# Optimization experiments

Measured on AMD Instinct MI355X. Metric: run time of the kernel, lower is better.

## Reference

```python
import jax, jax.numpy as jnp
import numpy as np

NL, D, Di, N, R, K, V, NH = 24, 768, 1536, 16, 48, 4, 50280, 12
BATCH, SEQ = 4, 256


def setup_inputs():
    key = jax.random.key(0)
    it = iter(jax.random.split(key, 48))
    g = lambda shape, s=0.02: jax.random.normal(next(it), shape, jnp.float32) * s
    inp = {
        "question_ids": jax.random.randint(next(it), (BATCH, SEQ), 0, V),
        "question_mask": jnp.ones((BATCH, SEQ), jnp.int32),
        "answer_ids": jax.random.randint(next(it), (BATCH, SEQ), 0, V),
        "answer_mask": jnp.ones((BATCH, SEQ), jnp.int32),
        "embed": g((V, D)),
        "norm_w": jnp.ones((NL, D)),
        "in_proj_w": g((NL, 2 * Di, D)),
        "conv_w": g((NL, Di, K), 0.1),
        "conv_b": jnp.zeros((NL, Di)),
        "x_proj_w": g((NL, R + 2 * N, Di)),
        "dt_proj_w": g((NL, Di, R)),
        "dt_proj_b": g((NL, Di), 0.5) - 4.0,
        "A_log": jnp.log(jnp.broadcast_to(jnp.arange(1, N + 1, dtype=jnp.float32), (NL, Di, N))) + 0.0,
        "D_p": jnp.ones((NL, Di)),
        "out_proj_w": g((NL, D, Di)),
        "norm_f": jnp.ones((D,)),
        "ln1_w": jnp.ones((D,)), "ln1_b": jnp.zeros((D,)),
        "qkv_w": g((3 * D, D)), "qkv_b": jnp.zeros((3 * D,)),
        "attn_out_w": g((D, D)), "attn_out_b": jnp.zeros((D,)),
        "ln2_w": jnp.ones((D,)), "ln2_b": jnp.zeros((D,)),
        "ff1_w": g((4 * D, D)), "ff1_b": jnp.zeros((4 * D,)),
        "ff2_w": g((D, 4 * D)), "ff2_b": jnp.zeros((D,)),
        "C_w": g((1, N)), "proj_out_w": g((D, Di)),
        "B_w": g((N, 1)), "proj_in_w": g((Di, D), 0.002),
    }
    return inp


def _rms(x, w, eps=1e-5):
    return x * jax.lax.rsqrt(jnp.mean(x * x, axis=-1, keepdims=True) + eps) * w


def _ln(x, w, b, eps=1e-5):
    m = jnp.mean(x, axis=-1, keepdims=True)
    v = jnp.var(x, axis=-1, keepdims=True)
    return (x - m) * jax.lax.rsqrt(v + eps) * w + b


def _mamba_block(h, layer, init_state):
    nw, ipw, cw, cb, xpw, dpw, dpb, alog, dp, opw = layer
    x_in = _rms(h, nw)
    xz = jnp.einsum('bld,ed->ble', x_in, ipw)  # (B,L,2*Di)
    x, z = jnp.split(xz, 2, axis=-1)
    L = x.shape[1]
    xp = jnp.pad(x, ((0, 0), (K - 1, 0), (0, 0)))  # causal depthwise conv, kernel K
    x = sum(xp[:, k:k + L, :] * cw[:, k] for k in range(K)) + cb
    x = jax.nn.silu(x)
    dbl = jnp.einsum('bld,ed->ble', x, xpw)
    dt, Bm, Cm = dbl[..., :R], dbl[..., R:R + N], dbl[..., R + N:]
    delta = jax.nn.softplus(jnp.einsum('blr,dr->bld', dt, dpw) + dpb)  # (B,L,Di)
    A = -jnp.exp(alog)  # (Di,N)

    def step(hs, t):  # selective scan, carry (B,Di,N)
        d_t, x_t, B_t, C_t = t
        hs = jnp.exp(d_t[..., None] * A) * hs + (d_t * x_t)[..., None] * B_t[:, None, :]
        return hs, jnp.einsum('bdn,bn->bd', hs, C_t)

    xs = tuple(jnp.moveaxis(a, 1, 0) for a in (delta, x, Bm, Cm))
    last, ys = jax.lax.scan(step, init_state, xs)
    y = jnp.moveaxis(ys, 0, 1) + x * dp
    y = y * jax.nn.silu(z)
    return h + jnp.einsum('bld,od->blo', y, opw), last


def _backbone(ids, mask, embed, mamba_params, norm_f, init_states):
    h = embed[ids] * mask[..., None].astype(embed.dtype)
    block = jax.checkpoint(_mamba_block)  # remat per layer: bounds bwd memory

    def layer_step(carry, xs):
        *layer, st = xs
        return block(carry, tuple(layer), st)

    h, lasts = jax.lax.scan(layer_step, h, mamba_params + (init_states,))
    h = _rms(h, norm_f)
    return jnp.einsum('bld,vd->blv', h, embed), lasts  # tied lm head


def _tf_layer(x, ln1_w, ln1_b, qkv_w, qkv_b, attn_out_w, attn_out_b, ln2_w, ln2_b, ff1_w, ff1_b, ff2_w, ff2_b):
    B, S, _ = x.shape
    hd = D // NH
    y = _ln(x, ln1_w, ln1_b)  # norm_first pre-LN
    q, k, v = jnp.split(y @ qkv_w.T + qkv_b, 3, axis=-1)
    q = q.reshape(B, S, NH, hd); k = k.reshape(B, S, NH, hd); v = v.reshape(B, S, NH, hd)
    att = jax.nn.softmax(jnp.einsum('bqhd,bkhd->bhqk', q, k) / jnp.sqrt(jnp.float32(hd)), axis=-1)
    o = jnp.einsum('bhqk,bkhd->bqhd', att, v).reshape(B, S, D)
    x = x + o @ attn_out_w.T + attn_out_b
    y = _ln(x, ln2_w, ln2_b)
    return x + jax.nn.gelu(y @ ff1_w.T + ff1_b, approximate=False) @ ff2_w.T + ff2_b


def _refine(states, C_w, proj_out_w, B_w, proj_in_w, tf_params):
    # states: (B, NL, Di, N); 12-step recurrent state refinement
    for _ in range(12):
        d = jnp.einsum('bsdn,n->bsd', states, C_w[0])  # C: Linear(16,1), squeeze(-1)
        d = jnp.einsum('bsd,od->bso', d, proj_out_w)   # 1536 -> 768
        d = _tf_layer(d, *tf_params)
        d = jnp.einsum('bso,do->bsd', d, proj_in_w)    # 768 -> 1536
        states = states + d[..., None] * B_w[:, 0]     # B: Linear(1,16)
    return states


def reference(question_ids, question_mask, answer_ids, answer_mask, embed, norm_w, in_proj_w, conv_w, conv_b, x_proj_w, dt_proj_w, dt_proj_b, A_log, D_p, out_proj_w, norm_f, ln1_w, ln1_b, qkv_w, qkv_b, attn_out_w, attn_out_b, ln2_w, ln2_b, ff1_w, ff1_b, ff2_w, ff2_b, C_w, proj_out_w, B_w, proj_in_w):
    mamba_params = (norm_w, in_proj_w, conv_w, conv_b, x_proj_w, dt_proj_w, dt_proj_b, A_log, D_p, out_proj_w)
    tf_params = (ln1_w, ln1_b, qkv_w, qkv_b, attn_out_w, attn_out_b, ln2_w, ln2_b, ff1_w, ff1_b, ff2_w, ff2_b)
    Bsz = question_ids.shape[0]
    zeros = jnp.zeros((NL, Bsz, Di, N), embed.dtype)
    _, lasts = _backbone(question_ids, question_mask, embed, mamba_params, norm_f, zeros)
    states = jnp.moveaxis(lasts, 0, 1)  # torch.stack(states, dim=1): (B, NL, Di, N)
    states = _refine(states, C_w, proj_out_w, B_w, proj_in_w, tf_params)
    logits, _ = _backbone(answer_ids, answer_mask, embed, mamba_params, norm_f, jnp.moveaxis(states, 0, 1))
    return logits
```

## Files before the change

### kernel.cpp

```cpp
#include <hip/hip_runtime.h>
#include <math.h>

namespace {

constexpr int kNL = 24, kD = 768, kDi = 1536, kN = 16, kR = 48, kK = 4, kV = 50280, kNH = 12;
constexpr int kB = 4, kS = 256;
constexpr int kMtok = kB * kS;
constexpr int kMref = kB * kNL;
constexpr int kVp = 50304;

using bf16x8   = __attribute__((ext_vector_type(8))) short;
using f32x4    = __attribute__((ext_vector_type(4))) float;
using ushort8v = __attribute__((ext_vector_type(8))) unsigned short;

__device__ __forceinline__ float siluf(float x) { return x / (1.f + __expf(-x)); }

__device__ __forceinline__ ushort f2b(float f) {
    union { float f; unsigned u; } v; v.f = f;
    unsigned u = v.u;
    unsigned r = (u + 0x7FFFu + ((u >> 16) & 1u)) >> 16;
    return (ushort)r;
}
__device__ __forceinline__ float b2f(ushort u) {
    union { unsigned u; float f; } v; v.u = (unsigned)u << 16; return v.f;
}

#define GLOAD_LDS(g, l) \
    __builtin_amdgcn_global_load_lds((const __attribute__((address_space(1))) void*)(g), \
                                     (__attribute__((address_space(3))) void*)(l), 16, 0, 0)

template <int BM, int BN, int BIAS, int ACT, int RES, int OUTMODE, int PIPE, int SSQ = 0>
__global__ __launch_bounds__(256, (PIPE == 3 ? 3 : 2)) void gemm_bf16(
    const ushort* __restrict__ A, int lda,
    const ushort* __restrict__ B, int ldb,
    float* __restrict__ C, int ldc,
    ushort* __restrict__ Cbf, int ldcb,
    float* __restrict__ C2,
    const float* __restrict__ bias,
    const float* __restrict__ aux,
    int M, int N, int K)
{
    constexpr int ACH = BM / 32;
    constexpr int BCH = BN / 32;
    constexpr int MI  = BM / 32;
    constexpr int NJ  = BN / 32;

    __shared__ ushort As[PIPE][BM * 64];
    __shared__ ushort Bs[PIPE][BN * 64];

    const int tid  = threadIdx.x;
    const int lane = tid & 63;
    const int wave = tid >> 6;
    const int m0 = blockIdx.y * BM;
    const int n0 = blockIdx.x * BN;
    const int wr = (wave >> 1) * (BM / 2);
    const int wc = (wave & 1) * (BN / 2);

    f32x4 acc[MI][NJ];
#pragma unroll
    for (int i = 0; i < MI; ++i)
#pragma unroll
        for (int j = 0; j < NJ; ++j) acc[i][j] = f32x4{0.f, 0.f, 0.f, 0.f};

    const int srow = lane >> 3;
    const int scol = ((lane & 7) ^ srow) * 8;
    const ushort* gA[ACH];
    const ushort* gB[BCH];
#pragma unroll
    for (int g = 0; g < ACH; ++g)
        gA[g] = A + (size_t)(m0 + (g * 4 + wave) * 8 + srow) * lda + scol;
#pragma unroll
    for (int g = 0; g < BCH; ++g)
        gB[g] = B + (size_t)(n0 + (g * 4 + wave) * 8 + srow) * ldb + scol;

    const int frow = lane & 15;
    const int kh   = lane >> 4;
    const int nt   = K >> 6;

    auto stage = [&](int t, int buf) {
        const int off = t * 64;
#pragma unroll
        for (int g = 0; g < ACH; ++g) GLOAD_LDS(gA[g] + off, &As[buf][(g * 4 + wave) * 512]);
#pragma unroll
        for (int g = 0; g < BCH; ++g) GLOAD_LDS(gB[g] + off, &Bs[buf][(g * 4 + wave) * 512]);
    };
    auto compute = [&](int buf) {
#pragma unroll
        for (int s = 0; s < 2; ++s) {
            bf16x8 fa[MI], fb[NJ];
#pragma unroll
            for (int i = 0; i < MI; ++i) {
                int r = wr + i * 16 + frow;
                int slot = (s * 4 + kh) ^ (r & 7);
                fa[i] = *(const bf16x8*)&As[buf][r * 64 + slot * 8];
            }
#pragma unroll
            for (int j = 0; j < NJ; ++j) {
                int r = wc + j * 16 + frow;
                int slot = (s * 4 + kh) ^ (r & 7);
                fb[j] = *(const bf16x8*)&Bs[buf][r * 64 + slot * 8];
            }
#pragma unroll
            for (int i = 0; i < MI; ++i)
#pragma unroll
                for (int j = 0; j < NJ; ++j)
                    acc[i][j] = __builtin_amdgcn_mfma_f32_16x16x32_bf16(fa[i], fb[j], acc[i][j], 0, 0, 0);
        }
    };

    if constexpr (PIPE == 3) {
        stage(0, 0);
        if (nt > 1) stage(1, 1);
        for (int t = 0; t < nt; ++t) {
            if (t < nt - 1) {
                asm volatile("s_waitcnt vmcnt(%0)" :: "n"(ACH + BCH) : "memory");
            } else {
                asm volatile("s_waitcnt vmcnt(0)" ::: "memory");
            }
            __builtin_amdgcn_s_barrier();
            if (t + 2 < nt) stage(t + 2, (t + 2) % 3);
            compute(t % 3);
        }
        __builtin_amdgcn_s_barrier();
    } else {
        stage(0, 0);
        __syncthreads();
        int cur = 0;
        for (int t = 0; t < nt; ++t) {
            if (t + 1 < nt) stage(t + 1, cur ^ 1);
            compute(cur);
            __syncthreads();
            cur ^= 1;
        }
    }

    const int ccol = lane & 15;
    const int crow = (lane >> 4) * 4;
    float rsq[MI][4];
    if constexpr (SSQ) {
#pragma unroll
        for (int i = 0; i < MI; ++i)
#pragma unroll
            for (int q = 0; q < 4; ++q) rsq[i][q] = 0.f;
    }
#pragma unroll
    for (int i = 0; i < MI; ++i) {
#pragma unroll
        for (int j = 0; j < NJ; ++j) {
            int gn = n0 + wc + j * 16 + ccol;
            if (gn >= N) continue;
            float bv = BIAS ? bias[gn] : 0.f;
#pragma unroll
            for (int q = 0; q < 4; ++q) {
                int gm = m0 + wr + i * 16 + crow + q;
                if (gm >= M) continue;
                float v = acc[i][j][q] + bv;
                if (ACT == 1) v = fmaxf(v, 0.f) + log1pf(expf(-fabsf(v)));
                if (ACT == 2) v = 0.5f * v * (1.f + erff(v * 0.70710678118654752f));
                if (OUTMODE == 3) {
                    if (gn < 48) Cbf[(size_t)gm * 64 + gn] = f2b(v);
                    else if (gn < 64) { Cbf[(size_t)gm * 64 + gn] = 0; C2[(size_t)(gn - 48) * kMtok + gm] = v; }
                    else if (gn < 80) C2[(size_t)(gn - 48) * kMtok + gm] = v;
                } else if (OUTMODE == 4) {
                    ((ushort*)C2)[(size_t)gn * kMtok + gm] = f2b(v);
                } else if (OUTMODE == 7) {
                    int bb = gm / kNL, ss = gm - bb * kNL;
                    float* stp = C2 + ((size_t)(ss * kB + bb) * kDi + gn) * kN;
                    float a2 = 0.f;
#pragma unroll
                    for (int nn = 0; nn < kN; ++nn) {
                        float sv = stp[nn] + v * bias[nn];
                        stp[nn] = sv;
                        a2 += sv * aux[nn];
                    }
                    Cbf[(size_t)gm * ldcb + gn] = f2b(a2);
                } else {
                    size_t ci = (size_t)gm * ldc + gn;
                    if (RES) v += C[ci];
                    if (OUTMODE != 2) C[ci] = v;
                    if (OUTMODE == 1 || OUTMODE == 2) Cbf[(size_t)gm * ldcb + gn] = f2b(v);
                    if constexpr (SSQ) rsq[i][q] += v * v;
                }
            }
        }
    }
    if constexpr (SSQ) {
#pragma unroll
        for (int i = 0; i < MI; ++i)
#pragma unroll
            for (int q = 0; q < 4; ++q) {
                rsq[i][q] += __shfl_xor(rsq[i][q], 1, 16);
                rsq[i][q] += __shfl_xor(rsq[i][q], 2, 16);
                rsq[i][q] += __shfl_xor(rsq[i][q], 4, 16);
                rsq[i][q] += __shfl_xor(rsq[i][q], 8, 16);
            }
        float* red = (float*)&As[0][0];
        __syncthreads();
        if ((lane & 15) == 0) {
#pragma unroll
            for (int i = 0; i < MI; ++i)
#pragma unroll
                for (int q = 0; q < 4; ++q) {
                    int rl = (wave >> 1) * 32 + i * 16 + (lane >> 4) * 4 + q;
                    red[(wave & 1) * 64 + rl] = rsq[i][q];
                }
        }
        __syncthreads();
        if (tid < 64) C2[(size_t)blockIdx.x * kMtok + m0 + tid] = red[tid] + red[64 + tid];
    }
}

template <int BM, int BN, int BIAS, int ACT, int RES, int OUTMODE, int PIPE, int SSQ = 0>
static void gemm(const ushort* A, int lda, const ushort* B, int ldb,
                 float* C, int ldc, ushort* Cb, int ldcb, float* C2,
                 const float* bias, const float* aux, int M, int N, int K, hipStream_t s)
{
    dim3 g((N + BN - 1) / BN, (M + BM - 1) / BM);
    gemm_bf16<BM, BN, BIAS, ACT, RES, OUTMODE, PIPE, SSQ><<<g, dim3(256), 0, s>>>(
        A, lda, B, ldb, C, ldc, Cb, ldcb, C2, bias, aux, M, N, K);
}

__global__ __launch_bounds__(256, 4) void gemm_rms(
    const float* __restrict__ hbuf, const float* __restrict__ ssq,
    const float* __restrict__ nw,
    const ushort* __restrict__ B, int ldb,
    ushort* __restrict__ Xbf, ushort* __restrict__ zTb,
    int M, int N, int K)
{
    constexpr int MI = 2, NJ = 2, BCH = 2;
    __shared__ ushort As[2][64 * 64];
    __shared__ ushort Bs[2][64 * 64];
    const int tid  = threadIdx.x;
    const int lane = tid & 63;
    const int wave = tid >> 6;
    const int m0 = blockIdx.y * 64;
    const int n0 = blockIdx.x * 64;
    const int wr = (wave >> 1) * 32;
    const int wc = (wave & 1) * 32;

    f32x4 acc[MI][NJ];
#pragma unroll
    for (int i = 0; i < MI; ++i)
#pragma unroll
        for (int j = 0; j < NJ; ++j) acc[i][j] = f32x4{0.f, 0.f, 0.f, 0.f};

    const int srow = lane >> 3;
    const int scol = ((lane & 7) ^ srow) * 8;
    const ushort* gB[BCH];
#pragma unroll
    for (int g = 0; g < BCH; ++g)
        gB[g] = B + (size_t)(n0 + (g * 4 + wave) * 8 + srow) * ldb + scol;

    int arow[2];
    float rs[2];
#pragma unroll
    for (int g = 0; g < 2; ++g) {
        arow[g] = m0 + (g * 4 + wave) * 8 + srow;
        float s = 0.f;
#pragma unroll
        for (int c = 0; c < 12; ++c) s += ssq[c * kMtok + arow[g]];
        rs[g] = rsqrtf(s * (1.f / 768.f) + 1e-5f);
    }

    const int frow = lane & 15;
    const int kh   = lane >> 4;
    const int nt   = K >> 6;

    float4 av[2][2], wv[2];
    auto loadA = [&](int t) {
        int k = t * 64 + scol;
        wv[0] = *(const float4*)&nw[k];
        wv[1] = *(const float4*)&nw[k + 4];
#pragma unroll
        for (int g = 0; g < 2; ++g) {
            av[g][0] = *(const float4*)&hbuf[(size_t)arow[g] * K + k];
            av[g][1] = *(const float4*)&hbuf[(size_t)arow[g] * K + k + 4];
        }
    };
    auto writeA = [&](int buf) {
#pragma unroll
        for (int g = 0; g < 2; ++g) {
            ushort8v o;
            o[0] = f2b(av[g][0].x * rs[g] * wv[0].x);
            o[1] = f2b(av[g][0].y * rs[g] * wv[0].y);
            o[2] = f2b(av[g][0].z * rs[g] * wv[0].z);
            o[3] = f2b(av[g][0].w * rs[g] * wv[0].w);
            o[4] = f2b(av[g][1].x * rs[g] * wv[1].x);
            o[5] = f2b(av[g][1].y * rs[g] * wv[1].y);
            o[6] = f2b(av[g][1].z * rs[g] * wv[1].z);
            o[7] = f2b(av[g][1].w * rs[g] * wv[1].w);
            *(ushort8v*)&As[buf][(g * 4 + wave) * 512 + lane * 8] = o;
        }
    };
    auto stageB = [&](int t, int buf) {
#pragma unroll
        for (int g = 0; g < BCH; ++g) GLOAD_LDS(gB[g] + t * 64, &Bs[buf][(g * 4 + wave) * 512]);
    };
    auto compute = [&](int buf) {
#pragma unroll
        for (int s = 0; s < 2; ++s) {
            bf16x8 fa[MI], fb[NJ];
#pragma unroll
            for (int i = 0; i < MI; ++i) {
                int r = wr + i * 16 + frow;
                int slot = (s * 4 + kh) ^ (r & 7);
                fa[i] = *(const bf16x8*)&As[buf][r * 64 + slot * 8];
            }
#pragma unroll
            for (int j = 0; j < NJ; ++j) {
                int r = wc + j * 16 + frow;
                int slot = (s * 4 + kh) ^ (r & 7);
                fb[j] = *(const bf16x8*)&Bs[buf][r * 64 + slot * 8];
            }
#pragma unroll
            for (int i = 0; i < MI; ++i)
#pragma unroll
                for (int j = 0; j < NJ; ++j)
                    acc[i][j] = __builtin_amdgcn_mfma_f32_16x16x32_bf16(fa[i], fb[j], acc[i][j], 0, 0, 0);
        }
    };

    loadA(0);
    stageB(0, 0);
    writeA(0);
    __syncthreads();
    int cur = 0;
    for (int t = 0; t < nt; ++t) {
        if (t + 1 < nt) { loadA(t + 1); stageB(t + 1, cur ^ 1); }
        compute(cur);
        if (t + 1 < nt) writeA(cur ^ 1);
        __syncthreads();
        cur ^= 1;
    }

    const int ccol = lane & 15;
    const int crow = (lane >> 4) * 4;
#pragma unroll
    for (int i = 0; i < MI; ++i) {
#pragma unroll
        for (int j = 0; j < NJ; ++j) {
            int gn = n0 + wc + j * 16 + ccol;
#pragma unroll
            for (int q = 0; q < 4; ++q) {
                int gm = m0 + wr + i * 16 + crow + q;
                float v = acc[i][j][q];
                if (gn < kDi) Xbf[(size_t)gm * kDi + gn] = f2b(v);
                else zTb[(size_t)(gn - kDi) * kMtok + gm] = f2b(siluf(v));
            }
        }
    }
}

__global__ void cvt_kernel(const float* __restrict__ src, ushort* __restrict__ dst, int n) {
    int i = (blockIdx.x * 256 + threadIdx.x) * 4;
    if (i >= n) return;
    float4 v = *(const float4*)(src + i);
    ushort4 o; o.x = f2b(v.x); o.y = f2b(v.y); o.z = f2b(v.z); o.w = f2b(v.w);
    *(ushort4*)(dst + i) = o;
}

__global__ void cvt_xpw_kernel(const float* __restrict__ src, ushort* __restrict__ dst) {
    int i = (blockIdx.x * 256 + threadIdx.x) * 4;
    if (i >= 24 * 80 * 1536) return;
    int l = i / (80 * 1536), r = i - l * (80 * 1536);
    int row = r / 1536, col = r - row * 1536;
    float4 v = *(const float4*)(src + i);
    ushort4 o; o.x = f2b(v.x); o.y = f2b(v.y); o.z = f2b(v.z); o.w = f2b(v.w);
    *(ushort4*)(dst + ((size_t)(l * 128 + row)) * 1536 + col) = o;
}

__global__ void cvt_dpw_kernel(const float* __restrict__ src, ushort* __restrict__ dst) {
    int i = blockIdx.x * 256 + threadIdx.x;
    if (i >= 24 * 1536 * 64) return;
    int col = i & 63, row = i >> 6;
    dst[i] = (col < 48) ? f2b(src[(size_t)row * 48 + col]) : (ushort)0;
}

__global__ void embed_kernel(const int* __restrict__ ids, const int* __restrict__ msk,
                             const float* __restrict__ embed, float* __restrict__ h,
                             float* __restrict__ ssq)
{
    int i = blockIdx.x * 256 + threadIdx.x;
    int row = i / kD, col = i - row * kD;
    float v = embed[(size_t)ids[row] * kD + col] * (float)msk[row];
    h[i] = v;
    float s = v * v;
    s += __shfl_xor(s, 1);  s += __shfl_xor(s, 2);  s += __shfl_xor(s, 4);
    s += __shfl_xor(s, 8);  s += __shfl_xor(s, 16); s += __shfl_xor(s, 32);
    if ((threadIdx.x & 63) == 0) ssq[(col >> 6) * kMtok + row] = s;
}

__global__ __launch_bounds__(256) void rms_kernel(const float* __restrict__ x,
                                                  const float* __restrict__ w,
                                                  ushort* __restrict__ out)
{
    __shared__ float red[256];
    int row = blockIdx.x, tid = threadIdx.x;
    const float* xr = x + (size_t)row * kD;
    float s = 0.f;
    for (int j = tid; j < kD; j += 256) { float v = xr[j]; s += v * v; }
    red[tid] = s; __syncthreads();
    for (int o = 128; o > 0; o >>= 1) { if (tid < o) red[tid] += red[tid + o]; __syncthreads(); }
    float rs = rsqrtf(red[0] / (float)kD + 1e-5f);
    for (int j = tid; j < kD; j += 256) out[(size_t)row * kD + j] = f2b(xr[j] * rs * w[j]);
}

__global__ __launch_bounds__(256) void ln_kernel(const float* __restrict__ x,
                                                 const float* __restrict__ w,
                                                 const float* __restrict__ b,
                                                 ushort* __restrict__ out)
{
    __shared__ float r1[256], r2[256];
    int row = blockIdx.x, tid = threadIdx.x;
    const float* xr = x + (size_t)row * kD;
    float s = 0.f, s2 = 0.f;
    for (int j = tid; j < kD; j += 256) { float v = xr[j]; s += v; s2 += v * v; }
    r1[tid] = s; r2[tid] = s2; __syncthreads();
    for (int o = 128; o > 0; o >>= 1) {
        if (tid < o) { r1[tid] += r1[tid + o]; r2[tid] += r2[tid + o]; }
        __syncthreads();
    }
    float mean = r1[0] / (float)kD;
    float var = r2[0] / (float)kD - mean * mean;
    float rsv = rsqrtf(var + 1e-5f);
    for (int j = tid; j < kD; j += 256)
        out[(size_t)row * kD + j] = f2b((xr[j] - mean) * rsv * w[j] + b[j]);
}

__global__ __launch_bounds__(256) void conv_kernel(
    const ushort* __restrict__ xb, const float* __restrict__ cw,
    const float* __restrict__ cb, ushort* __restrict__ xc_bf,
    ushort* __restrict__ xcT)
{
    int d   = blockIdx.x * 256 + threadIdx.x;
    int bt0 = blockIdx.y * 16;
    int t0  = bt0 & (kS - 1);
    float w0 = cw[d * 4], w1 = cw[d * 4 + 1], w2 = cw[d * 4 + 2], w3 = cw[d * 4 + 3];
    float bias = cb[d];
    float xv[19];
#pragma unroll
    for (int j = 0; j < 19; ++j) {
        int tt = t0 - 3 + j;
        xv[j] = (tt >= 0) ? b2f(xb[(size_t)(bt0 - 3 + j) * kDi + d]) : 0.f;
    }
    ushort8v o0, o1;
#pragma unroll
    for (int e = 0; e < 16; ++e) {
        float s = bias + xv[e] * w0 + xv[e + 1] * w1 + xv[e + 2] * w2 + xv[e + 3] * w3;
        ushort us = f2b(siluf(s));
        xc_bf[(size_t)(bt0 + e) * kDi + d] = us;
        if (e < 8) o0[e] = us; else o1[e - 8] = us;
    }
    *(ushort8v*)(xcT + (size_t)d * kMtok + bt0)     = o0;
    *(ushort8v*)(xcT + (size_t)d * kMtok + bt0 + 8) = o1;
}

__global__ __launch_bounds__(256) void scan_kernel(
    const ushort* __restrict__ dltT, const ushort* __restrict__ xcT,
    const ushort* __restrict__ zT, const float* __restrict__ bcT,
    const float* __restrict__ alog, const float* __restrict__ dp,
    float* __restrict__ states, ushort* __restrict__ y)
{
    int gid = blockIdx.x * 256 + threadIdx.x;
    int n = gid & 15;
    int d = (gid >> 4) % kDi;
    int b = gid / (kDi * kN);
    float Areg = -__expf(alog[d * kN + n]);
    float dpv = dp[d];
    size_t sidx = (size_t)(b * kDi + d) * kN + n;
    float hs = states[sidx];
    const ushort8v* pD = (const ushort8v*)(dltT + (size_t)d * kMtok + b * kS);
    const ushort8v* pX = (const ushort8v*)(xcT  + (size_t)d * kMtok + b * kS);
    const ushort8v* pZ = (const ushort8v*)(zT   + (size_t)d * kMtok + b * kS);
    const float4* pB = (const float4*)(bcT + (size_t)n * kMtok + b * kS);
    const float4* pC = (const float4*)(bcT + (size_t)(16 + n) * kMtok + b * kS);
    ushort8v D = pD[0], X = pX[0], Z = pZ[0];
    float4 B0 = pB[0], B1 = pB[1], C0 = pC[0], C1 = pC[1];
    ushort* yrow = y + (size_t)(b * kS) * kDi + d;
    for (int g = 0; g < kS / 8; ++g) {
        ushort8v Dn, Xn, Zn; float4 Bn0, Bn1, Cn0, Cn1;
        if (g + 1 < kS / 8) {
            Dn = pD[g + 1]; Xn = pX[g + 1]; Zn = pZ[g + 1];
            Bn0 = pB[2 * g + 2]; Bn1 = pB[2 * g + 3];
            Cn0 = pC[2 * g + 2]; Cn1 = pC[2 * g + 3];
        }
#pragma unroll
        for (int e = 0; e < 8; ++e) {
            float dv = b2f(D[e]), xv = b2f(X[e]), zv = b2f(Z[e]);
            float Bv = (e < 4) ? (&B0.x)[e] : (&B1.x)[e - 4];
            float Cv = (e < 4) ? (&C0.x)[e] : (&C1.x)[e - 4];
            hs = __expf(dv * Areg) * hs + (dv * xv) * Bv;
            float p = hs * Cv;
            p += __shfl_xor(p, 1, 16);
            p += __shfl_xor(p, 2, 16);
            p += __shfl_xor(p, 4, 16);
            p += __shfl_xor(p, 8, 16);
            if (n == 0) yrow[(size_t)(g * 8 + e) * kDi] = f2b((p + xv * dpv) * zv);
        }
        D = Dn; X = Xn; Z = Zn; B0 = Bn0; B1 = Bn1; C0 = Cn0; C1 = Cn1;
    }
    states[sidx] = hs;
}

__global__ void contract_kernel(const float* __restrict__ st, const float* __restrict__ Cw,
                                ushort* __restrict__ dDi)
{
    int i = blockIdx.x * 256 + threadIdx.x;
    int row = i / kDi, di = i - row * kDi;
    int b = row / kNL, s = row - b * kNL;
    const float* sp = st + ((size_t)(s * kB + b) * kDi + di) * kN;
    float acc = 0.f;
#pragma unroll
    for (int nn = 0; nn < kN; ++nn) acc += sp[nn] * Cw[nn];
    dDi[i] = f2b(acc);
}

__global__ __launch_bounds__(32) void attn_kernel(const float* __restrict__ qkv,
                                                  ushort* __restrict__ o)
{
    int b = blockIdx.x / kNH;
    int hh = blockIdx.x - b * kNH;
    int sq = threadIdx.x;
    if (sq >= kNL) return;
    const float* qrow = qkv + (size_t)(b * kNL + sq) * (3 * kD) + hh * 64;
    float q[64];
#pragma unroll
    for (int e = 0; e < 64; ++e) q[e] = qrow[e];
    float sc[kNL];
    float mx = -1e30f;
    for (int sk = 0; sk < kNL; ++sk) {
        const float* krow = qkv + (size_t)(b * kNL + sk) * (3 * kD) + kD + hh * 64;
        float dt = 0.f;
#pragma unroll
        for (int e = 0; e < 64; ++e) dt += q[e] * krow[e];
        dt *= 0.125f;
        sc[sk] = dt;
        mx = fmaxf(mx, dt);
    }
    float sum = 0.f;
    for (int sk = 0; sk < kNL; ++sk) { sc[sk] = expf(sc[sk] - mx); sum += sc[sk]; }
    float inv = 1.f / sum;
    float out[64];
#pragma unroll
    for (int e = 0; e < 64; ++e) out[e] = 0.f;
    for (int sk = 0; sk < kNL; ++sk) {
        float wgt = sc[sk] * inv;
        const float* vrow = qkv + (size_t)(b * kNL + sk) * (3 * kD) + 2 * kD + hh * 64;
#pragma unroll
        for (int e = 0; e < 64; ++e) out[e] += wgt * vrow[e];
    }
    ushort* orow = o + (size_t)(b * kNL + sq) * kD + hh * 64;
#pragma unroll
    for (int e = 0; e < 64; ++e) orow[e] = f2b(out[e]);
}

}

extern "C" void kernel_launch(void* const* d_in, const int* in_sizes, int n_in,
                              void* d_out, int out_size, void* d_ws, size_t ws_size,
                              hipStream_t stream)
{
    const int*   q_ids  = (const int*)d_in[0];
    const int*   q_msk  = (const int*)d_in[1];
    const int*   a_ids  = (const int*)d_in[2];
    const int*   a_msk  = (const int*)d_in[3];
    const float* embed  = (const float*)d_in[4];
    const float* norm_w = (const float*)d_in[5];
    const float* ipw    = (const float*)d_in[6];
    const float* cw     = (const float*)d_in[7];
    const float* cb     = (const float*)d_in[8];
    const float* xpw    = (const float*)d_in[9];
    const float* dpw    = (const float*)d_in[10];
    const float* dpb    = (const float*)d_in[11];
    const float* alog   = (const float*)d_in[12];
    const float* dpp    = (const float*)d_in[13];
    const float* opw    = (const float*)d_in[14];
    const float* norm_f = (const float*)d_in[15];
    const float* ln1w   = (const float*)d_in[16];
    const float* ln1b   = (const float*)d_in[17];
    const float* qkvw   = (const float*)d_in[18];
    const float* qkvbi  = (const float*)d_in[19];
    const float* aow    = (const float*)d_in[20];
    const float* aob    = (const float*)d_in[21];
    const float* ln2w   = (const float*)d_in[22];
    const float* ln2b   = (const float*)d_in[23];
    const float* ff1w   = (const float*)d_in[24];
    const float* ff1b   = (const float*)d_in[25];
    const float* ff2w   = (const float*)d_in[26];
    const float* ff2b   = (const float*)d_in[27];
    const float* Cwp    = (const float*)d_in[28];
    const float* powp   = (const float*)d_in[29];
    const float* Bwp    = (const float*)d_in[30];
    const float* piwp   = (const float*)d_in[31];

    char* base = (char*)d_ws;
    size_t cur = 0;
    auto allocB = [&](size_t bytes) { char* p = base + cur; cur = (cur + bytes + 255) & ~(size_t)255; return p; };
    auto allocF = [&](size_t n) { return (float*)allocB(n * 4); };
    auto allocH = [&](size_t n) { return (ushort*)allocB(n * 2); };

    float* h     = allocF((size_t)kMtok * kD);
    float* ssqp  = allocF((size_t)12 * kMtok);
    float* bcT   = allocF((size_t)32 * kMtok);
    float* st    = allocF((size_t)kNL * kB * kDi * kN);
    float* x768  = allocF((size_t)kMref * kD);
    float* qkvB  = allocF((size_t)kMref * 3 * kD);
    ushort* x_bf    = allocH((size_t)kMtok * kDi);
    ushort* zT_b    = allocH((size_t)kDi * kMtok);
    ushort* xcT_b   = allocH((size_t)kDi * kMtok);
    ushort* dltT_b  = allocH((size_t)kDi * kMtok);
    ushort* xc_bf   = allocH((size_t)kMtok * kDi);
    ushort* dtin_bf = allocH((size_t)kMtok * 64);
    ushort* yb_bf   = allocH((size_t)kMtok * kDi);
    ushort* xin_bf  = allocH((size_t)kMtok * kD);
    ushort* dDi_bf  = allocH((size_t)128 * kDi);
    ushort* tb_bf   = allocH((size_t)128 * kD);
    ushort* o768_bf = allocH((size_t)128 * kD);
    ushort* f3_bf   = allocH((size_t)128 * 4 * kD);
    ushort* x768_bf = allocH((size_t)128 * kD);
    ushort* xpw_bf  = allocH((size_t)kNL * 128 * kDi);
    ushort* dpw_bf  = allocH((size_t)kNL * kDi * 64);
    ushort* powp_bf = allocH((size_t)kD * kDi);
    ushort* qkvw_bf = allocH((size_t)3 * kD * kD);
    ushort* aow_bf  = allocH((size_t)kD * kD);
    ushort* ff1w_bf = allocH((size_t)4 * kD * kD);
    ushort* ff2w_bf = allocH((size_t)kD * 4 * kD);
    ushort* piw_bf  = allocH((size_t)kDi * kD);
    ushort* emb_bf  = allocH((size_t)kVp * kD);

    size_t base_end = cur;
    ushort* ipw_all = allocH((size_t)kNL * 2 * kDi * kD);
    ushort* opw_all = allocH((size_t)kNL * kD * kDi);
    bool full = (cur <= ws_size);
    ushort* ipw_stg = nullptr;
    ushort* opw_stg = nullptr;
    if (!full) {
        cur = base_end;
        ipw_stg = allocH((size_t)2 * kDi * kD);
        opw_stg = allocH((size_t)kD * kDi);
        if (cur > ws_size) return;
    }

    auto cvt = [&](const float* s, ushort* d, size_t n) {
        cvt_kernel<<<dim3((unsigned)((n / 4 + 255) / 256)), dim3(256), 0, stream>>>(s, d, (int)n);
    };

    hipMemsetAsync(st, 0, sizeof(float) * (size_t)kNL * kB * kDi * kN, stream);

    cvt_xpw_kernel<<<dim3(2880), dim3(256), 0, stream>>>(xpw, xpw_bf);
    cvt_dpw_kernel<<<dim3(9216), dim3(256), 0, stream>>>(dpw, dpw_bf);
    cvt(powp, powp_bf, (size_t)kD * kDi);
    cvt(qkvw, qkvw_bf, (size_t)3 * kD * kD);
    cvt(aow,  aow_bf,  (size_t)kD * kD);
    cvt(ff1w, ff1w_bf, (size_t)4 * kD * kD);
    cvt(ff2w, ff2w_bf, (size_t)kD * 4 * kD);
    cvt(piwp, piw_bf,  (size_t)kDi * kD);
    cvt(embed, emb_bf, (size_t)kV * kD);
    if (full) {
        cvt(ipw, ipw_all, (size_t)kNL * 2 * kDi * kD);
        cvt(opw, opw_all, (size_t)kNL * kD * kDi);
    }

    for (int pass = 0; pass < 2; ++pass) {
        const int* ids = pass ? a_ids : q_ids;
        const int* msk = pass ? a_msk : q_msk;

        embed_kernel<<<dim3(kMtok * kD / 256), dim3(256), 0, stream>>>(ids, msk, embed, h, ssqp);

        for (int l = 0; l < kNL; ++l) {
            const ushort* ipw_l;
            const ushort* opw_l;
            if (full) {
                ipw_l = ipw_all + (size_t)l * 2 * kDi * kD;
                opw_l = opw_all + (size_t)l * kD * kDi;
            } else {
                cvt(ipw + (size_t)l * 2 * kDi * kD, ipw_stg, (size_t)2 * kDi * kD);
                cvt(opw + (size_t)l * kD * kDi, opw_stg, (size_t)kD * kDi);
                ipw_l = ipw_stg;
                opw_l = opw_stg;
            }
            gemm_rms<<<dim3(48, 16), dim3(256), 0, stream>>>(
                h, ssqp, norm_w + (size_t)l * kD, ipw_l, kD, x_bf, zT_b, kMtok, 2 * kDi, kD);
            conv_kernel<<<dim3(kDi / 256, kMtok / 16), dim3(256), 0, stream>>>(
                x_bf, cw + (size_t)l * kDi * kK, cb + (size_t)l * kDi, xc_bf, xcT_b);
            gemm<64, 64, 0, 0, 0, 3, 3>(xc_bf, kDi, xpw_bf + (size_t)l * 128 * kDi, kDi,
                                        nullptr, 0, dtin_bf, 0, bcT,
                                        nullptr, nullptr, kMtok, 128, kDi, stream);
            gemm<64, 64, 1, 1, 0, 4, 3>(dtin_bf, 64, dpw_bf + (size_t)l * kDi * 64, 64,
                                        nullptr, 0, nullptr, 0, (float*)dltT_b,
                                        dpb + (size_t)l * kDi, nullptr, kMtok, kDi, 64, stream);
            scan_kernel<<<dim3(kB * kDi * kN / 256), dim3(256), 0, stream>>>(
                dltT_b, xcT_b, zT_b, bcT, alog + (size_t)l * kDi * kN, dpp + (size_t)l * kDi,
                st + (size_t)l * kB * kDi * kN, yb_bf);
            gemm<64, 64, 0, 0, 1, 0, 3, 1>(yb_bf, kDi, opw_l, kDi, h, kD, nullptr, 0, ssqp,
                                           nullptr, nullptr, kMtok, kD, kDi, stream);
        }

        if (pass == 0) {
            contract_kernel<<<dim3(kMref * kDi / 256), dim3(256), 0, stream>>>(st, Cwp, dDi_bf);
            for (int it = 0; it < 12; ++it) {
                gemm<64, 64, 0, 0, 0, 0, 3>(dDi_bf, kDi, powp_bf, kDi, x768, kD, nullptr, 0, nullptr,
                                            nullptr, nullptr, kMref, kD, kDi, stream);
                ln_kernel<<<dim3(kMref), dim3(256), 0, stream>>>(x768, ln1w, ln1b, tb_bf);
                gemm<64, 64, 1, 0, 0, 0, 3>(tb_bf, kD, qkvw_bf, kD, qkvB, 3 * kD, nullptr, 0, nullptr,
                                            qkvbi, nullptr, kMref, 3 * kD, kD, stream);
                attn_kernel<<<dim3(kB * kNH), dim3(32), 0, stream>>>(qkvB, o768_bf);
                gemm<64, 64, 1, 0, 1, 0, 3>(o768_bf, kD, aow_bf, kD, x768, kD, nullptr, 0, nullptr,
                                            aob, nullptr, kMref, kD, kD, stream);
                ln_kernel<<<dim3(kMref), dim3(256), 0, stream>>>(x768, ln2w, ln2b, tb_bf);
                gemm<64, 64, 1, 2, 0, 2, 3>(tb_bf, kD, ff1w_bf, kD, nullptr, 0, f3_bf, 4 * kD, nullptr,
                                            ff1b, nullptr, kMref, 4 * kD, kD, stream);
                gemm<64, 64, 1, 0, 1, 1, 3>(f3_bf, 4 * kD, ff2w_bf, 4 * kD, x768, kD, x768_bf, kD, nullptr,
                                            ff2b, nullptr, kMref, kD, 4 * kD, stream);
                gemm<64, 64, 0, 0, 0, 7, 3>(x768_bf, kD, piw_bf, kD, nullptr, 0, dDi_bf, kDi, st,
                                            Bwp, Cwp, kMref, kDi, kD, stream);
            }
        } else {
            rms_kernel<<<dim3(kMtok), dim3(256), 0, stream>>>(h, norm_f, xin_bf);
            gemm<128, 128, 0, 0, 0, 0, 2>(xin_bf, kD, emb_bf, kD, (float*)d_out, kV, nullptr, 0, nullptr,
                                          nullptr, nullptr, kMtok, kV, kD, stream);
        }
    }
}
```

Before: 8.637 ms.

## Fuse conv, x_proj and dt_proj into one kernel; fold ff2 into proj_in

Adds a per-layer prep kernel that computes the causal conv with SiLU and the x_proj GEMM, then the dt_proj GEMM with softplus, all in one launch. This removes the conv_kernel and two GEMM launches along with their intermediate global buffers. In the refine loop it precomputes proj_in·ff2 and its bias offline and concatenates the activations into one wide K=3840 operand, so the ff2 GEMM and the proj_in GEMM become a single GEMM. The prep kernel launches only 32 blocks, which may underuse the GPU, and the folded weights change bf16 rounding.

```diff
diff --git a/kernel.cpp b/kernel.cpp
--- a/kernel.cpp
+++ b/kernel.cpp
@@ -8,6 +8,7 @@
 constexpr int kMtok = kB * kS;
 constexpr int kMref = kB * kNL;
 constexpr int kVp = 50304;
+constexpr int kKa = 3840;
 
 using bf16x8   = __attribute__((ext_vector_type(8))) short;
 using f32x4    = __attribute__((ext_vector_type(4))) float;
@@ -38,6 +39,7 @@
     float* __restrict__ C2,
     const float* __restrict__ bias,
     const float* __restrict__ aux,
+    const float* __restrict__ aux2,
     int M, int N, int K)
 {
     constexpr int ACH = BM / 32;
@@ -157,19 +159,13 @@
                 float v = acc[i][j][q] + bv;
                 if (ACT == 1) v = fmaxf(v, 0.f) + log1pf(expf(-fabsf(v)));
                 if (ACT == 2) v = 0.5f * v * (1.f + erff(v * 0.70710678118654752f));
-                if (OUTMODE == 3) {
-                    if (gn < 48) Cbf[(size_t)gm * 64 + gn] = f2b(v);
-                    else if (gn < 64) { Cbf[(size_t)gm * 64 + gn] = 0; C2[(size_t)(gn - 48) * kMtok + gm] = v; }
-                    else if (gn < 80) C2[(size_t)(gn - 48) * kMtok + gm] = v;
-                } else if (OUTMODE == 4) {
-                    ((ushort*)C2)[(size_t)gn * kMtok + gm] = f2b(v);
-                } else if (OUTMODE == 7) {
+                if (OUTMODE == 7) {
                     int bb = gm / kNL, ss = gm - bb * kNL;
                     float* stp = C2 + ((size_t)(ss * kB + bb) * kDi + gn) * kN;
                     float a2 = 0.f;
 #pragma unroll
                     for (int nn = 0; nn < kN; ++nn) {
-                        float sv = stp[nn] + v * bias[nn];
+                        float sv = stp[nn] + v * aux2[nn];
                         stp[nn] = sv;
                         a2 += sv * aux[nn];
                     }
@@ -213,11 +209,12 @@
 template <int BM, int BN, int BIAS, int ACT, int RES, int OUTMODE, int PIPE, int SSQ = 0>
 static void gemm(const ushort* A, int lda, const ushort* B, int ldb,
                  float* C, int ldc, ushort* Cb, int ldcb, float* C2,
-                 const float* bias, const float* aux, int M, int N, int K, hipStream_t s)
+                 const float* bias, const float* aux, int M, int N, int K, hipStream_t s,
+                 const float* aux2 = nullptr)
 {
     dim3 g((N + BN - 1) / BN, (M + BM - 1) / BM);
     gemm_bf16<BM, BN, BIAS, ACT, RES, OUTMODE, PIPE, SSQ><<<g, dim3(256), 0, s>>>(
-        A, lda, B, ldb, C, ldc, Cb, ldcb, C2, bias, aux, M, N, K);
+        A, lda, B, ldb, C, ldc, Cb, ldcb, C2, bias, aux, aux2, M, N, K);
 }
 
 __global__ __launch_bounds__(256, 4) void gemm_rms(
@@ -351,6 +348,205 @@
     }
 }
 
+__global__ __launch_bounds__(256, 2) void prep_kernel(
+    const ushort* __restrict__ xb,
+    const float* __restrict__ cw,
+    const float* __restrict__ cb,
+    const ushort* __restrict__ xpw128,
+    const ushort* __restrict__ dpw64,
+    const float* __restrict__ dpb,
+    ushort* __restrict__ xcT,
+    float*  __restrict__ bcT,
+    ushort* __restrict__ dltT)
+{
+    __shared__ ushort lds[2 * 32 * 64 + 2 * 128 * 64];
+    ushort* As1 = lds;
+    ushort* Bs1 = lds + 4096;
+    ushort* dtL = lds;
+    ushort* Bs2 = lds + 4096;
+
+    const int tid  = threadIdx.x;
+    const int lane = tid & 63;
+    const int wave = tid >> 6;
+    const int m0   = blockIdx.x * 32;
+
+    f32x4 acc[2][2];
+#pragma unroll
+    for (int i = 0; i < 2; ++i)
+#pragma unroll
+        for (int j = 0; j < 2; ++j) acc[i][j] = f32x4{0.f, 0.f, 0.f, 0.f};
+
+    const int srow = lane >> 3;
+    const int scol8 = ((lane & 7) ^ srow) * 8;
+    const int frow = lane & 15;
+    const int kh   = lane >> 4;
+    const int ccol = lane & 15;
+    const int crow = (lane >> 4) * 4;
+
+    const int ar = tid >> 3;
+    const int acg = tid & 7;
+    const int gt = m0 + ar;
+    const int tloc = gt & (kS - 1);
+
+    ushort8v xrow[4];
+    float4 w4[8];
+    float cbv[8];
+    auto loadA = [&](int t) {
+        int gcol = t * 64 + ((acg ^ (ar & 7)) << 3);
+#pragma unroll
+        for (int j = 0; j < 4; ++j) {
+            int tt = tloc - 3 + j;
+            if (tt >= 0) xrow[j] = *(const ushort8v*)&xb[(size_t)(gt - 3 + j) * kDi + gcol];
+            else { ushort8v z; for (int e = 0; e < 8; ++e) z[e] = 0; xrow[j] = z; }
+        }
+#pragma unroll
+        for (int e = 0; e < 8; ++e) w4[e] = *(const float4*)&cw[(size_t)(gcol + e) * 4];
+        float4 c0 = *(const float4*)&cb[gcol];
+        float4 c1 = *(const float4*)&cb[gcol + 4];
+        cbv[0] = c0.x; cbv[1] = c0.y; cbv[2] = c0.z; cbv[3] = c0.w;
+        cbv[4] = c1.x; cbv[5] = c1.y; cbv[6] = c1.z; cbv[7] = c1.w;
+    };
+    auto writeA = [&](int buf) {
+        ushort8v o;
+#pragma unroll
+        for (int e = 0; e < 8; ++e) {
+            float s = cbv[e] + b2f(xrow[0][e]) * w4[e].x + b2f(xrow[1][e]) * w4[e].y
+                             + b2f(xrow[2][e]) * w4[e].z + b2f(xrow[3][e]) * w4[e].w;
+            o[e] = f2b(siluf(s));
+        }
+        *(ushort8v*)&As1[buf * 2048 + ar * 64 + acg * 8] = o;
+    };
+    const ushort* gB[4];
+#pragma unroll
+    for (int g = 0; g < 4; ++g)
+        gB[g] = xpw128 + (size_t)((wave * 4 + g) * 8 + srow) * kDi + scol8;
+    auto stageB = [&](int t, int buf) {
+#pragma unroll
+        for (int g = 0; g < 4; ++g)
+            GLOAD_LDS(gB[g] + t * 64, &Bs1[buf * 8192 + (wave * 4 + g) * 512]);
+    };
+    auto compute1 = [&](int buf) {
+#pragma unroll
+        for (int s = 0; s < 2; ++s) {
+            bf16x8 fa[2], fb[2];
+#pragma unroll
+            for (int i = 0; i < 2; ++i) {
+                int r = i * 16 + frow;
+                int slot = (s * 4 + kh) ^ (r & 7);
+                fa[i] = *(const bf16x8*)&As1[buf * 2048 + r * 64 + slot * 8];
+            }
+#pragma unroll
+            for (int j = 0; j < 2; ++j) {
+                int rb = wave * 32 + j * 16 + frow;
+                int slot = (s * 4 + kh) ^ (rb & 7);
+                fb[j] = *(const bf16x8*)&Bs1[buf * 8192 + rb * 64 + slot * 8];
+            }
+#pragma unroll
+            for (int i = 0; i < 2; ++i)
+#pragma unroll
+                for (int j = 0; j < 2; ++j)
+                    acc[i][j] = __builtin_amdgcn_mfma_f32_16x16x32_bf16(fa[i], fb[j], acc[i][j], 0, 0, 0);
+        }
+    };
+    auto xcTwrite = [&](int buf, int t) {
+        int d = lane;
+        ushort vals[8];
+#pragma unroll
+        for (int u = 0; u < 8; ++u) {
+            int r = wave * 8 + u;
+            vals[u] = As1[buf * 2048 + r * 64 + (((d >> 3) ^ (r & 7)) * 8) + (d & 7)];
+        }
+        ushort8v o;
+#pragma unroll
+        for (int u = 0; u < 8; ++u) o[u] = vals[u];
+        *(ushort8v*)&xcT[(size_t)(t * 64 + d) * kMtok + m0 + wave * 8] = o;
+    };
+
+    loadA(0);
+    stageB(0, 0);
+    writeA(0);
+    __syncthreads();
+    int cur = 0;
+    for (int t = 0; t < 24; ++t) {
+        if (t + 1 < 24) { loadA(t + 1); stageB(t + 1, cur ^ 1); }
+        compute1(cur);
+        xcTwrite(cur, t);
+        if (t + 1 < 24) writeA(cur ^ 1);
+        __syncthreads();
+        cur ^= 1;
+    }
+
+#pragma unroll
+    for (int i = 0; i < 2; ++i) {
+#pragma unroll
+        for (int j = 0; j < 2; ++j) {
+            int gnl = wave * 32 + j * 16 + ccol;
+#pragma unroll
+            for (int q = 0; q < 4; ++q) {
+                int rl = i * 16 + crow + q;
+                float v = acc[i][j][q];
+                if (gnl < 64)
+                    dtL[rl * 64 + (((gnl >> 3) ^ (rl & 7)) * 8) + (gnl & 7)] = (gnl < 48) ? f2b(v) : (ushort)0;
+                if (gnl >= 48 && gnl < 80)
+                    bcT[(size_t)(gnl - 48) * kMtok + m0 + rl] = v;
+            }
+        }
+    }
+    __syncthreads();
+
+    const ushort* gB2[2];
+#pragma unroll
+    for (int g = 0; g < 2; ++g)
+        gB2[g] = dpw64 + (size_t)((wave * 2 + g) * 8 + srow) * 64 + scol8;
+    auto stage2 = [&](int n, int buf) {
+#pragma unroll
+        for (int g = 0; g < 2; ++g)
+            GLOAD_LDS(gB2[g] + (size_t)n * 64 * 64, &Bs2[buf * 4096 + (wave * 2 + g) * 512]);
+    };
+
+    stage2(0, 0);
+    __syncthreads();
+    int cur2 = 0;
+    for (int n = 0; n < 24; ++n) {
+        if (n + 1 < 24) stage2(n + 1, cur2 ^ 1);
+        f32x4 a2[2];
+        a2[0] = f32x4{0.f, 0.f, 0.f, 0.f};
+        a2[1] = f32x4{0.f, 0.f, 0.f, 0.f};
+#pragma unroll
+        for (int s = 0; s < 2; ++s) {
+            bf16x8 fa[2], fb;
+#pragma unroll
+            for (int i = 0; i < 2; ++i) {
+                int r = i * 16 + frow;
+                int slot = (s * 4 + kh) ^ (r & 7);
+                fa[i] = *(const bf16x8*)&dtL[r * 64 + slot * 8];
+            }
+            int rb = wave * 16 + frow;
+            int slot = (s * 4 + kh) ^ (rb & 7);
+            fb = *(const bf16x8*)&Bs2[cur2 * 4096 + rb * 64 + slot * 8];
+#pragma unroll
+            for (int i = 0; i < 2; ++i)
+                a2[i] = __builtin_amdgcn_mfma_f32_16x16x32_bf16(fa[i], fb, a2[i], 0, 0, 0);
+        }
+#pragma unroll
+        for (int i = 0; i < 2; ++i) {
+            int gn = n * 64 + wave * 16 + ccol;
+            float bv = dpb[gn];
+            ushort ov[4];
+#pragma unroll
+            for (int q = 0; q < 4; ++q) {
+                float v = a2[i][q] + bv;
+                v = fmaxf(v, 0.f) + log1pf(expf(-fabsf(v)));
+                ov[q] = f2b(v);
+            }
+            *(ushort4*)&dltT[(size_t)gn * kMtok + m0 + i * 16 + crow] =
+                make_ushort4(ov[0], ov[1], ov[2], ov[3]);
+        }
+        __syncthreads();
+        cur2 ^= 1;
+    }
+}
+
 __global__ void cvt_kernel(const float* __restrict__ src, ushort* __restrict__ dst, int n) {
     int i = (blockIdx.x * 256 + threadIdx.x) * 4;
     if (i >= n) return;
@@ -374,6 +570,29 @@
     if (i >= 24 * 1536 * 64) return;
     int col = i & 63, row = i >> 6;
     dst[i] = (col < 48) ? f2b(src[(size_t)row * 48 + col]) : (ushort)0;
+}
+
+__global__ void cvt_ff2T_kernel(const float* __restrict__ src, ushort* __restrict__ dst) {
+    int i = blockIdx.x * 256 + threadIdx.x;
+    if (i >= 768 * 3072) return;
+    int d = i / 3072, f = i - d * 3072;
+    dst[(size_t)f * 768 + d] = f2b(src[i]);
+}
+
+__global__ void cvt_pi_kernel(const float* __restrict__ src, ushort* __restrict__ dst) {
+    int i = blockIdx.x * 256 + threadIdx.x;
+    if (i >= 1536 * 768) return;
+    int o = i / 768, d = i - o * 768;
+    dst[(size_t)o * kKa + d] = f2b(src[i]);
+}
+
+__global__ void pib_kernel(const float* __restrict__ piw, const float* __restrict__ ff2b,
+                           float* __restrict__ bias2) {
+    int o = blockIdx.x * 256 + threadIdx.x;
+    if (o >= 1536) return;
+    float s = 0.f;
+    for (int d = 0; d < 768; ++d) s += piw[(size_t)o * 768 + d] * ff2b[d];
+    bias2[o] = s;
 }
 
 __global__ void embed_kernel(const int* __restrict__ ids, const int* __restrict__ msk,
@@ -425,34 +644,6 @@
     float rsv = rsqrtf(var + 1e-5f);
     for (int j = tid; j < kD; j += 256)
         out[(size_t)row * kD + j] = f2b((xr[j] - mean) * rsv * w[j] + b[j]);
-}
-
-__global__ __launch_bounds__(256) void conv_kernel(
-    const ushort* __restrict__ xb, const float* __restrict__ cw,
-    const float* __restrict__ cb, ushort* __restrict__ xc_bf,
-    ushort* __restrict__ xcT)
-{
-    int d   = blockIdx.x * 256 + threadIdx.x;
-    int bt0 = blockIdx.y * 16;
-    int t0  = bt0 & (kS - 1);
-    float w0 = cw[d * 4], w1 = cw[d * 4 + 1], w2 = cw[d * 4 + 2], w3 = cw[d * 4 + 3];
-    float bias = cb[d];
-    float xv[19];
-#pragma unroll
-    for (int j = 0; j < 19; ++j) {
-        int tt = t0 - 3 + j;
-        xv[j] = (tt >= 0) ? b2f(xb[(size_t)(bt0 - 3 + j) * kDi + d]) : 0.f;
-    }
-    ushort8v o0, o1;
-#pragma unroll
-    for (int e = 0; e < 16; ++e) {
-        float s = bias + xv[e] * w0 + xv[e + 1] * w1 + xv[e + 2] * w2 + xv[e + 3] * w3;
-        ushort us = f2b(siluf(s));
-        xc_bf[(size_t)(bt0 + e) * kDi + d] = us;
-        if (e < 8) o0[e] = us; else o1[e - 8] = us;
-    }
-    *(ushort8v*)(xcT + (size_t)d * kMtok + bt0)     = o0;
-    *(ushort8v*)(xcT + (size_t)d * kMtok + bt0 + 8) = o1;
 }
 
 __global__ __launch_bounds__(256) void scan_kernel(
@@ -605,27 +796,26 @@
     float* st    = allocF((size_t)kNL * kB * kDi * kN);
     float* x768  = allocF((size_t)kMref * kD);
     float* qkvB  = allocF((size_t)kMref * 3 * kD);
+    float* bias2 = allocF((size_t)kDi);
     ushort* x_bf    = allocH((size_t)kMtok * kDi);
     ushort* zT_b    = allocH((size_t)kDi * kMtok);
     ushort* xcT_b   = allocH((size_t)kDi * kMtok);
     ushort* dltT_b  = allocH((size_t)kDi * kMtok);
-    ushort* xc_bf   = allocH((size_t)kMtok * kDi);
-    ushort* dtin_bf = allocH((size_t)kMtok * 64);
     ushort* yb_bf   = allocH((size_t)kMtok * kDi);
     ushort* xin_bf  = allocH((size_t)kMtok * kD);
     ushort* dDi_bf  = allocH((size_t)128 * kDi);
     ushort* tb_bf   = allocH((size_t)128 * kD);
     ushort* o768_bf = allocH((size_t)128 * kD);
-    ushort* f3_bf   = allocH((size_t)128 * 4 * kD);
-    ushort* x768_bf = allocH((size_t)128 * kD);
+    ushort* A2      = allocH((size_t)128 * kKa);
     ushort* xpw_bf  = allocH((size_t)kNL * 128 * kDi);
     ushort* dpw_bf  = allocH((size_t)kNL * kDi * 64);
     ushort* powp_bf = allocH((size_t)kD * kDi);
     ushort* qkvw_bf = allocH((size_t)3 * kD * kD);
     ushort* aow_bf  = allocH((size_t)kD * kD);
     ushort* ff1w_bf = allocH((size_t)4 * kD * kD);
-    ushort* ff2w_bf = allocH((size_t)kD * 4 * kD);
+    ushort* ff2wT   = allocH((size_t)4 * kD * kD);
     ushort* piw_bf  = allocH((size_t)kDi * kD);
+    ushort* B2      = allocH((size_t)kDi * kKa);
     ushort* emb_bf  = allocH((size_t)kVp * kD);
 
     size_t base_end = cur;
@@ -653,8 +843,12 @@
     cvt(qkvw, qkvw_bf, (size_t)3 * kD * kD);
     cvt(aow,  aow_bf,  (size_t)kD * kD);
     cvt(ff1w, ff1w_bf, (size_t)4 * kD * kD);
-    cvt(ff2w, ff2w_bf, (size_t)kD * 4 * kD);
     cvt(piwp, piw_bf,  (size_t)kDi * kD);
+    cvt_ff2T_kernel<<<dim3(9216), dim3(256), 0, stream>>>(ff2w, ff2wT);
+    cvt_pi_kernel<<<dim3(4608), dim3(256), 0, stream>>>(piwp, B2);
+    pib_kernel<<<dim3(6), dim3(256), 0, stream>>>(piwp, ff2b, bias2);
+    gemm<64, 64, 0, 0, 0, 2, 3>(piw_bf, kD, ff2wT, kD, nullptr, 0, B2 + kD, kKa, nullptr,
+                                nullptr, nullptr, kDi, 4 * kD, kD, stream);
     cvt(embed, emb_bf, (size_t)kV * kD);
     if (full) {
         cvt(ipw, ipw_all, (size_t)kNL * 2 * kDi * kD);
@@ -681,14 +875,10 @@
             }
             gemm_rms<<<dim3(48, 16), dim3(256), 0, stream>>>(
                 h, ssqp, norm_w + (size_t)l * kD, ipw_l, kD, x_bf, zT_b, kMtok, 2 * kDi, kD);
-            conv_kernel<<<dim3(kDi / 256, kMtok / 16), dim3(256), 0, stream>>>(
-                x_bf, cw + (size_t)l * kDi * kK, cb + (size_t)l * kDi, xc_bf, xcT_b);
-            gemm<64, 64, 0, 0, 0, 3, 3>(xc_bf, kDi, xpw_bf + (size_t)l * 128 * kDi, kDi,
-                                        nullptr, 0, dtin_bf, 0, bcT,
-                                        nullptr, nullptr, kMtok, 128, kDi, stream);
-            gemm<64, 64, 1, 1, 0, 4, 3>(dtin_bf, 64, dpw_bf + (size_t)l * kDi * 64, 64,
-                                        nullptr, 0, nullptr, 0, (float*)dltT_b,
-                                        dpb + (size_t)l * kDi, nullptr, kMtok, kDi, 64, stream);
+            prep_kernel<<<dim3(32), dim3(256), 0, stream>>>(
+                x_bf, cw + (size_t)l * kDi * kK, cb + (size_t)l * kDi,
+                xpw_bf + (size_t)l * 128 * kDi, dpw_bf + (size_t)l * kDi * 64,
+                dpb + (size_t)l * kDi, xcT_b, bcT, dltT_b);
             scan_kernel<<<dim3(kB * kDi * kN / 256), dim3(256), 0, stream>>>(
                 dltT_b, xcT_b, zT_b, bcT, alog + (size_t)l * kDi * kN, dpp + (size_t)l * kDi,
                 st + (size_t)l * kB * kDi * kN, yb_bf);
@@ -705,15 +895,13 @@
                 gemm<64, 64, 1, 0, 0, 0, 3>(tb_bf, kD, qkvw_bf, kD, qkvB, 3 * kD, nullptr, 0, nullptr,
                                             qkvbi, nullptr, kMref, 3 * kD, kD, stream);
                 attn_kernel<<<dim3(kB * kNH), dim3(32), 0, stream>>>(qkvB, o768_bf);
-                gemm<64, 64, 1, 0, 1, 0, 3>(o768_bf, kD, aow_bf, kD, x768, kD, nullptr, 0, nullptr,
+                gemm<64, 64, 1, 0, 1, 1, 3>(o768_bf, kD, aow_bf, kD, x768, kD, A2, kKa, nullptr,
                                             aob, nullptr, kMref, kD, kD, stream);
                 ln_kernel<<<dim3(kMref), dim3(256), 0, stream>>>(x768, ln2w, ln2b, tb_bf);
-                gemm<64, 64, 1, 2, 0, 2, 3>(tb_bf, kD, ff1w_bf, kD, nullptr, 0, f3_bf, 4 * kD, nullptr,
+                gemm<64, 64, 1, 2, 0, 2, 3>(tb_bf, kD, ff1w_bf, kD, nullptr, 0, A2 + kD, kKa, nullptr,
                                             ff1b, nullptr, kMref, 4 * kD, kD, stream);
-                gemm<64, 64, 1, 0, 1, 1, 3>(f3_bf, 4 * kD, ff2w_bf, 4 * kD, x768, kD, x768_bf, kD, nullptr,
-                                            ff2b, nullptr, kMref, kD, 4 * kD, stream);
-                gemm<64, 64, 0, 0, 0, 7, 3>(x768_bf, kD, piw_bf, kD, nullptr, 0, dDi_bf, kDi, st,
-                                            Bwp, Cwp, kMref, kDi, kD, stream);
+                gemm<64, 64, 1, 0, 0, 7, 3>(A2, kKa, B2, kKa, nullptr, 0, dDi_bf, kDi, st,
+                                            bias2, Cwp, kMref, kDi, kKa, stream, Bwp);
             }
         } else {
             rms_kernel<<<dim3(kMtok), dim3(256), 0, stream>>>(h, norm_f, xin_bf);
```

After: 11.85 ms. 37.2% more time.
